# Kernel tuning notes

Measured on AMD Instinct MI355X. Metric: run time of the kernel, lower is better.

## Reference

```python
import jax, jax.numpy as jnp
import numpy as np
import math

H = 768          # bert hidden size
N_HYPO = 384     # number of hyponym instance embeddings
N_HYPER = 384    # number of hypernym instance embeddings
NUM_LABELS = 3


def setup_inputs() -> dict:
    key = jax.random.key(0)
    k1, k2, k3 = jax.random.split(key, 3)
    return {
        "hypo_embeddings": jax.random.normal(k1, (N_HYPO, H), dtype=jnp.float32),
        "hyper_embeddings": jax.random.normal(k2, (N_HYPER, H), dtype=jnp.float32),
        "W_cls": jax.random.normal(k3, (NUM_LABELS, 4 * H), dtype=jnp.float32) * 0.02,
        "b_cls": jnp.zeros((NUM_LABELS,), dtype=jnp.float32),
    }


def reference(hypo_embeddings, hyper_embeddings, W_cls, b_cls):
    h = hypo_embeddings.shape[-1]
    inv_sqrt_h = 1.0 / math.sqrt(h)
    # elementwise outer-product attention score: tanh(x_i * y_j) summed over hidden
    # [n_hypo, n_hyper, h] intermediate -> [n_hypo, n_hyper]
    att = jnp.tanh(hypo_embeddings[:, None, :] * hyper_embeddings[None, :, :]).sum(-1) * inv_sqrt_h

    hypo_side_att = jax.nn.softmax(att, axis=-1)   # rows attend over hypers
    hyper_side_att = jax.nn.softmax(att, axis=0)   # cols attend over hypos

    hyper_typ = hypo_side_att.sum(axis=0)
    hyper_typ = hyper_typ / hyper_typ.sum()
    hypo_typ = hyper_side_att.sum(axis=-1)
    hypo_typ = hypo_typ / hypo_typ.sum()

    # typicalness-weighted prototype pooling
    hyper_prototype = jnp.einsum('nm,md,n->d', hypo_side_att, hyper_embeddings, hypo_typ)
    hypo_prototype = jnp.einsum('nm,nd,m->d', hyper_side_att, hypo_embeddings, hyper_typ)

    feats = jnp.concatenate([
        hyper_prototype,
        hypo_prototype,
        hyper_prototype - hypo_prototype,
        hyper_prototype * hypo_prototype,
    ])  # [4h]
    sub_pred = W_cls @ feats + b_cls  # [num_labels]
    return sub_pred
```

## Files before the change

kernel.cpp:

```cpp
#include <hip/hip_runtime.h>
#include <hip/hip_bf16.h>

#define NN 384
#define HH 768
#define HP 772
#define L2E 1.4426950408889634f
#define TWO_L2E 2.8853900817779268f
#define INV_SQRT_H 0.03608439182435161f

__device__ __forceinline__ float exp2_hw(float x) { return __builtin_amdgcn_exp2f(x); }
__device__ __forceinline__ float rcp_hw(float x) { return __builtin_amdgcn_rcpf(x); }

__global__ __launch_bounds__(256) void k_att(const float* __restrict__ X,
                                             const float* __restrict__ Y,
                                             float* __restrict__ att) {
    __shared__ float xs[8 * HP];
    __shared__ float ys[8 * HP];
    __shared__ float part[4][64];
    const int tid = threadIdx.x;
    const int i0 = blockIdx.y * 8, j0 = blockIdx.x * 8;

    const float4* gx = (const float4*)(X + i0 * HH);
    const float4* gy = (const float4*)(Y + j0 * HH);
#pragma unroll
    for (int p = 0; p < 6; p++) {
        int e = tid + p * 256;
        int r = e / 192, c = e - r * 192;
        float4 vx = gx[e];
        float4 vy = gy[e];
        ((float4*)(xs + r * HP))[c] = vx;
        vy.x *= TWO_L2E; vy.y *= TWO_L2E; vy.z *= TWO_L2E; vy.w *= TWO_L2E;
        ((float4*)(ys + r * HP))[c] = vy;
    }
    __syncthreads();

    const int wv = tid >> 6, ln = tid & 63;
    const int i = ln >> 3, j = ln & 7;
    const float4* xr = (const float4*)(xs + i * HP) + wv * 48;
    const float4* yr = (const float4*)(ys + j * HP) + wv * 48;
    float a0 = 0.f, a1 = 0.f, a2 = 0.f, a3 = 0.f;
#pragma unroll 8
    for (int m = 0; m < 48; m++) {
        float4 a = xr[m];
        float4 b = yr[m];
        a0 += rcp_hw(exp2_hw(a.x * b.x) + 1.f);
        a1 += rcp_hw(exp2_hw(a.y * b.y) + 1.f);
        a2 += rcp_hw(exp2_hw(a.z * b.z) + 1.f);
        a3 += rcp_hw(exp2_hw(a.w * b.w) + 1.f);
    }
    part[wv][ln] = (a0 + a1) + (a2 + a3);
    __syncthreads();
    if (tid < 64) {
        float s = part[0][tid] + part[1][tid] + part[2][tid] + part[3][tid];
        int ii = tid >> 3, jj = tid & 7;
        att[(i0 + ii) * NN + (j0 + jj)] = (768.f - 2.f * s) * INV_SQRT_H;
    }
}

__global__ __launch_bounds__(256) void k_stats(const float* __restrict__ att, float* rowM,
                                               float* rowRS, float* colM, float* colRS) {
    __shared__ float red[4];
    int b = blockIdx.x, t = threadIdx.x;
    bool isRow = b < NN;
    int x = isRow ? b : b - NN;
    float a0 = isRow ? att[x * NN + t] : att[t * NN + x];
    float a1 = (t < 128) ? (isRow ? att[x * NN + t + 256] : att[(t + 256) * NN + x]) : -1e30f;
    float m = fmaxf(a0, a1);
#pragma unroll
    for (int o = 32; o; o >>= 1) m = fmaxf(m, __shfl_xor(m, o, 64));
    if ((t & 63) == 0) red[t >> 6] = m;
    __syncthreads();
    float M = fmaxf(fmaxf(red[0], red[1]), fmaxf(red[2], red[3]));
    __syncthreads();
    float s = exp2_hw((a0 - M) * L2E);
    if (t < 128) s += exp2_hw((a1 - M) * L2E);
#pragma unroll
    for (int o = 32; o; o >>= 1) s += __shfl_xor(s, o, 64);
    if ((t & 63) == 0) red[t >> 6] = s;
    __syncthreads();
    if (t == 0) {
        float S = (red[0] + red[1]) + (red[2] + red[3]);
        if (isRow) { rowM[x] = M; rowRS[x] = 1.f / S; }
        else       { colM[x] = M; colRS[x] = 1.f / S; }
    }
}

__global__ __launch_bounds__(256) void k_typ(const float* __restrict__ att,
                                             const float* __restrict__ rowM,
                                             const float* __restrict__ rowRS,
                                             const float* __restrict__ colM,
                                             const float* __restrict__ colRS,
                                             float* hyper_typ, float* hypo_typ) {
    __shared__ float red[4];
    int b = blockIdx.x, t = threadIdx.x;
    bool isCol = b < NN;
    int x = isCol ? b : b - NN;
    float s = 0.f;
    if (isCol) {
        int j = x;
        for (int i = t; i < NN; i += 256)
            s += exp2_hw((att[i * NN + j] - rowM[i]) * L2E) * rowRS[i];
    } else {
        int i = x;
        for (int j = t; j < NN; j += 256)
            s += exp2_hw((att[i * NN + j] - colM[j]) * L2E) * colRS[j];
    }
#pragma unroll
    for (int o = 32; o; o >>= 1) s += __shfl_xor(s, o, 64);
    if ((t & 63) == 0) red[t >> 6] = s;
    __syncthreads();
    if (t == 0) {
        float S = (red[0] + red[1]) + (red[2] + red[3]);
        if (isCol) hyper_typ[x] = S * (1.f / NN);
        else       hypo_typ[x]  = S * (1.f / NN);
    }
}

__global__ __launch_bounds__(256) void k_w(const float* __restrict__ att,
                                           const float* __restrict__ rowM,
                                           const float* __restrict__ rowRS,
                                           const float* __restrict__ colM,
                                           const float* __restrict__ colRS,
                                           const float* __restrict__ hypo_typ,
                                           const float* __restrict__ hyper_typ,
                                           float* w_hyper, float* w_hypo) {
    __shared__ float red[4];
    int b = blockIdx.x, t = threadIdx.x;
    bool isCol = b < NN;
    int x = isCol ? b : b - NN;
    float s = 0.f;
    if (isCol) {
        int j = x;
        for (int i = t; i < NN; i += 256)
            s += exp2_hw((att[i * NN + j] - rowM[i]) * L2E) * rowRS[i] * hypo_typ[i];
    } else {
        int i = x;
        for (int j = t; j < NN; j += 256)
            s += exp2_hw((att[i * NN + j] - colM[j]) * L2E) * colRS[j] * hyper_typ[j];
    }
#pragma unroll
    for (int o = 32; o; o >>= 1) s += __shfl_xor(s, o, 64);
    if ((t & 63) == 0) red[t >> 6] = s;
    __syncthreads();
    if (t == 0) {
        float S = (red[0] + red[1]) + (red[2] + red[3]);
        if (isCol) w_hyper[x] = S;
        else       w_hypo[x]  = S;
    }
}

__global__ __launch_bounds__(256) void k_proto(const float* __restrict__ X,
                                               const float* __restrict__ Y,
                                               const float* __restrict__ w_hyper,
                                               const float* __restrict__ w_hypo,
                                               float* hp, float* hq) {
    __shared__ float red[4][64];
    int b = blockIdx.x, t = threadIdx.x;
    bool hyper = b < 12;
    int bb = hyper ? b : b - 12;
    int dl = t & 63, w = t >> 6;
    int d = bb * 64 + dl;
    float s = 0.f;
    if (hyper) {
        for (int j = w * 96; j < w * 96 + 96; j++) s += w_hyper[j] * Y[j * HH + d];
    } else {
        for (int i = w * 96; i < w * 96 + 96; i++) s += w_hypo[i] * X[i * HH + d];
    }
    red[w][dl] = s;
    __syncthreads();
    if (t < 64) {
        float S = red[0][t] + red[1][t] + red[2][t] + red[3][t];
        if (hyper) hp[bb * 64 + t] = S;
        else       hq[bb * 64 + t] = S;
    }
}

__global__ __launch_bounds__(256) void k_cls(const float* __restrict__ W,
                                             const float* __restrict__ bias,
                                             const float* __restrict__ hp,
                                             const float* __restrict__ hq,
                                             float* __restrict__ out) {
    __shared__ float red[3][4];
    int t = threadIdx.x;
    float acc0 = 0.f, acc1 = 0.f, acc2 = 0.f;
    for (int d = t; d < 4 * HH; d += 256) {
        int seg = d / HH, r = d - seg * HH;
        float f = (seg == 0) ? hp[r] : (seg == 1) ? hq[r] : (seg == 2) ? (hp[r] - hq[r]) : (hp[r] * hq[r]);
        acc0 += W[d] * f;
        acc1 += W[3072 + d] * f;
        acc2 += W[6144 + d] * f;
    }
#pragma unroll
    for (int o = 32; o; o >>= 1) {
        acc0 += __shfl_xor(acc0, o, 64);
        acc1 += __shfl_xor(acc1, o, 64);
        acc2 += __shfl_xor(acc2, o, 64);
    }
    if ((t & 63) == 0) {
        red[0][t >> 6] = acc0;
        red[1][t >> 6] = acc1;
        red[2][t >> 6] = acc2;
    }
    __syncthreads();
    if (t < 3) {
        float S = red[t][0] + red[t][1] + red[t][2] + red[t][3] + bias[t];
        out[t] = S;
    }
}

extern "C" void kernel_launch(void* const* d_in, const int* in_sizes, int n_in,
                              void* d_out, int out_size, void* d_ws, size_t ws_size,
                              hipStream_t stream) {
    const float* X = (const float*)d_in[0];
    const float* Y = (const float*)d_in[1];
    const float* W = (const float*)d_in[2];
    const float* B = (const float*)d_in[3];
    float* out = (float*)d_out;

    float* ws = (float*)d_ws;
    float* att       = ws;
    float* rowM      = att + NN * NN;
    float* rowRS     = rowM + NN;
    float* colM      = rowRS + NN;
    float* colRS     = colM + NN;
    float* hyper_typ = colRS + NN;
    float* hypo_typ  = hyper_typ + NN;
    float* w_hyper   = hypo_typ + NN;
    float* w_hypo    = w_hyper + NN;
    float* hp        = w_hypo + NN;
    float* hq        = hp + HH;

    k_att<<<dim3(48, 48), 256, 0, stream>>>(X, Y, att);
    k_stats<<<768, 256, 0, stream>>>(att, rowM, rowRS, colM, colRS);
    k_typ<<<768, 256, 0, stream>>>(att, rowM, rowRS, colM, colRS, hyper_typ, hypo_typ);
    k_w<<<768, 256, 0, stream>>>(att, rowM, rowRS, colM, colRS, hypo_typ, hyper_typ, w_hyper, w_hypo);
    k_proto<<<24, 256, 0, stream>>>(X, Y, w_hyper, w_hypo, hp, hq);
    k_cls<<<1, 256, 0, stream>>>(W, B, hp, hq, out);
}
```

Baseline: 103.2 us.

## Fuse post-attention stages into one persistent kernel with grid barriers

Replaces the five kernels after the score computation (stats, typicalness, weights, prototypes, classifier) with a single 384-block kernel that separates phases with atomic-counter grid barriers. The score kernel now also writes a transposed copy of the matrix, so column reductions become contiguous row reads. The aim is to remove four launch gaps and the strided column accesses. In exchange it adds a second full matrix write, relies on all 384 blocks being co-resident for the spin barriers, and resets the barrier counters from one block of the score kernel.

```diff
diff --git a/kernel.cpp b/kernel.cpp
--- a/kernel.cpp
+++ b/kernel.cpp
@@ -13,12 +13,16 @@
 
 __global__ __launch_bounds__(256) void k_att(const float* __restrict__ X,
                                              const float* __restrict__ Y,
-                                             float* __restrict__ att) {
+                                             float* __restrict__ att,
+                                             float* __restrict__ attT,
+                                             unsigned* __restrict__ bar) {
     __shared__ float xs[8 * HP];
     __shared__ float ys[8 * HP];
     __shared__ float part[4][64];
     const int tid = threadIdx.x;
     const int i0 = blockIdx.y * 8, j0 = blockIdx.x * 8;
+
+    if (blockIdx.x == 0 && blockIdx.y == 0) bar[tid] = 0u;
 
     const float4* gx = (const float4*)(X + i0 * HH);
     const float4* gy = (const float4*)(Y + j0 * HH);
@@ -53,158 +57,141 @@
     if (tid < 64) {
         float s = part[0][tid] + part[1][tid] + part[2][tid] + part[3][tid];
         int ii = tid >> 3, jj = tid & 7;
-        att[(i0 + ii) * NN + (j0 + jj)] = (768.f - 2.f * s) * INV_SQRT_H;
-    }
-}
-
-__global__ __launch_bounds__(256) void k_stats(const float* __restrict__ att, float* rowM,
-                                               float* rowRS, float* colM, float* colRS) {
-    __shared__ float red[4];
-    int b = blockIdx.x, t = threadIdx.x;
-    bool isRow = b < NN;
-    int x = isRow ? b : b - NN;
-    float a0 = isRow ? att[x * NN + t] : att[t * NN + x];
-    float a1 = (t < 128) ? (isRow ? att[x * NN + t + 256] : att[(t + 256) * NN + x]) : -1e30f;
-    float m = fmaxf(a0, a1);
+        float v = (768.f - 2.f * s) * INV_SQRT_H;
+        att[(i0 + ii) * NN + (j0 + jj)] = v;
+        attT[(j0 + jj) * NN + (i0 + ii)] = v;
+    }
+}
+
+__device__ __forceinline__ float blk_sum(float v, float* tmp) {
 #pragma unroll
-    for (int o = 32; o; o >>= 1) m = fmaxf(m, __shfl_xor(m, o, 64));
-    if ((t & 63) == 0) red[t >> 6] = m;
-    __syncthreads();
-    float M = fmaxf(fmaxf(red[0], red[1]), fmaxf(red[2], red[3]));
-    __syncthreads();
-    float s = exp2_hw((a0 - M) * L2E);
-    if (t < 128) s += exp2_hw((a1 - M) * L2E);
+    for (int o = 32; o; o >>= 1) v += __shfl_xor(v, o, 64);
+    int t = threadIdx.x;
+    if ((t & 63) == 0) tmp[t >> 6] = v;
+    __syncthreads();
+    float r = (tmp[0] + tmp[1]) + (tmp[2] + tmp[3]);
+    __syncthreads();
+    return r;
+}
+__device__ __forceinline__ float blk_max(float v, float* tmp) {
 #pragma unroll
-    for (int o = 32; o; o >>= 1) s += __shfl_xor(s, o, 64);
-    if ((t & 63) == 0) red[t >> 6] = s;
-    __syncthreads();
-    if (t == 0) {
-        float S = (red[0] + red[1]) + (red[2] + red[3]);
-        if (isRow) { rowM[x] = M; rowRS[x] = 1.f / S; }
-        else       { colM[x] = M; colRS[x] = 1.f / S; }
-    }
-}
-
-__global__ __launch_bounds__(256) void k_typ(const float* __restrict__ att,
-                                             const float* __restrict__ rowM,
-                                             const float* __restrict__ rowRS,
-                                             const float* __restrict__ colM,
-                                             const float* __restrict__ colRS,
-                                             float* hyper_typ, float* hypo_typ) {
-    __shared__ float red[4];
-    int b = blockIdx.x, t = threadIdx.x;
-    bool isCol = b < NN;
-    int x = isCol ? b : b - NN;
-    float s = 0.f;
-    if (isCol) {
-        int j = x;
-        for (int i = t; i < NN; i += 256)
-            s += exp2_hw((att[i * NN + j] - rowM[i]) * L2E) * rowRS[i];
-    } else {
-        int i = x;
-        for (int j = t; j < NN; j += 256)
-            s += exp2_hw((att[i * NN + j] - colM[j]) * L2E) * colRS[j];
-    }
-#pragma unroll
-    for (int o = 32; o; o >>= 1) s += __shfl_xor(s, o, 64);
-    if ((t & 63) == 0) red[t >> 6] = s;
-    __syncthreads();
-    if (t == 0) {
-        float S = (red[0] + red[1]) + (red[2] + red[3]);
-        if (isCol) hyper_typ[x] = S * (1.f / NN);
-        else       hypo_typ[x]  = S * (1.f / NN);
-    }
-}
-
-__global__ __launch_bounds__(256) void k_w(const float* __restrict__ att,
-                                           const float* __restrict__ rowM,
-                                           const float* __restrict__ rowRS,
-                                           const float* __restrict__ colM,
-                                           const float* __restrict__ colRS,
-                                           const float* __restrict__ hypo_typ,
-                                           const float* __restrict__ hyper_typ,
-                                           float* w_hyper, float* w_hypo) {
-    __shared__ float red[4];
-    int b = blockIdx.x, t = threadIdx.x;
-    bool isCol = b < NN;
-    int x = isCol ? b : b - NN;
-    float s = 0.f;
-    if (isCol) {
-        int j = x;
-        for (int i = t; i < NN; i += 256)
-            s += exp2_hw((att[i * NN + j] - rowM[i]) * L2E) * rowRS[i] * hypo_typ[i];
-    } else {
-        int i = x;
-        for (int j = t; j < NN; j += 256)
-            s += exp2_hw((att[i * NN + j] - colM[j]) * L2E) * colRS[j] * hyper_typ[j];
-    }
-#pragma unroll
-    for (int o = 32; o; o >>= 1) s += __shfl_xor(s, o, 64);
-    if ((t & 63) == 0) red[t >> 6] = s;
-    __syncthreads();
-    if (t == 0) {
-        float S = (red[0] + red[1]) + (red[2] + red[3]);
-        if (isCol) w_hyper[x] = S;
-        else       w_hypo[x]  = S;
-    }
-}
-
-__global__ __launch_bounds__(256) void k_proto(const float* __restrict__ X,
-                                               const float* __restrict__ Y,
-                                               const float* __restrict__ w_hyper,
-                                               const float* __restrict__ w_hypo,
-                                               float* hp, float* hq) {
+    for (int o = 32; o; o >>= 1) v = fmaxf(v, __shfl_xor(v, o, 64));
+    int t = threadIdx.x;
+    if ((t & 63) == 0) tmp[t >> 6] = v;
+    __syncthreads();
+    float r = fmaxf(fmaxf(tmp[0], tmp[1]), fmaxf(tmp[2], tmp[3]));
+    __syncthreads();
+    return r;
+}
+
+__device__ __forceinline__ void grid_bar(unsigned* bar, int idx, unsigned nb) {
+    __syncthreads();
+    if (threadIdx.x == 0) {
+        unsigned* cnt = bar + idx * 64;
+        unsigned* flg = cnt + 32;
+        __threadfence();
+        unsigned old = atomicAdd(cnt, 1u);
+        if (old == nb - 1u) {
+            atomicExch(flg, 1u);
+        } else {
+            while (atomicAdd(flg, 0u) == 0u) { __builtin_amdgcn_s_sleep(2); }
+        }
+        __threadfence();
+    }
+    __syncthreads();
+}
+
+__global__ __launch_bounds__(256) void k_tail(const float* __restrict__ att,
+                                              const float* __restrict__ attT,
+                                              const float* __restrict__ X,
+                                              const float* __restrict__ Y,
+                                              const float* __restrict__ W,
+                                              const float* __restrict__ bias,
+                                              float* rowM, float* rowRS, float* colM, float* colRS,
+                                              float* hyper_typ, float* hypo_typ,
+                                              float* w_hyper, float* w_hypo,
+                                              float* hp, float* hq,
+                                              unsigned* bar, float* out) {
+    __shared__ float tmp[4];
     __shared__ float red[4][64];
-    int b = blockIdx.x, t = threadIdx.x;
-    bool hyper = b < 12;
-    int bb = hyper ? b : b - 12;
-    int dl = t & 63, w = t >> 6;
-    int d = bb * 64 + dl;
-    float s = 0.f;
-    if (hyper) {
-        for (int j = w * 96; j < w * 96 + 96; j++) s += w_hyper[j] * Y[j * HH + d];
-    } else {
-        for (int i = w * 96; i < w * 96 + 96; i++) s += w_hypo[i] * X[i * HH + d];
-    }
-    red[w][dl] = s;
-    __syncthreads();
-    if (t < 64) {
-        float S = red[0][t] + red[1][t] + red[2][t] + red[3][t];
-        if (hyper) hp[bb * 64 + t] = S;
-        else       hq[bb * 64 + t] = S;
-    }
-}
-
-__global__ __launch_bounds__(256) void k_cls(const float* __restrict__ W,
-                                             const float* __restrict__ bias,
-                                             const float* __restrict__ hp,
-                                             const float* __restrict__ hq,
-                                             float* __restrict__ out) {
-    __shared__ float red[3][4];
-    int t = threadIdx.x;
-    float acc0 = 0.f, acc1 = 0.f, acc2 = 0.f;
-    for (int d = t; d < 4 * HH; d += 256) {
-        int seg = d / HH, r = d - seg * HH;
-        float f = (seg == 0) ? hp[r] : (seg == 1) ? hq[r] : (seg == 2) ? (hp[r] - hq[r]) : (hp[r] * hq[r]);
-        acc0 += W[d] * f;
-        acc1 += W[3072 + d] * f;
-        acc2 += W[6144 + d] * f;
-    }
-#pragma unroll
-    for (int o = 32; o; o >>= 1) {
-        acc0 += __shfl_xor(acc0, o, 64);
-        acc1 += __shfl_xor(acc1, o, 64);
-        acc2 += __shfl_xor(acc2, o, 64);
-    }
-    if ((t & 63) == 0) {
-        red[0][t >> 6] = acc0;
-        red[1][t >> 6] = acc1;
-        red[2][t >> 6] = acc2;
-    }
-    __syncthreads();
-    if (t < 3) {
-        float S = red[t][0] + red[t][1] + red[t][2] + red[t][3] + bias[t];
-        out[t] = S;
+    const int b = blockIdx.x, t = threadIdx.x;
+    const unsigned nb = gridDim.x;
+
+    {
+        float a0 = att[b * NN + t];
+        float a1 = (t < 128) ? att[b * NN + 256 + t] : -1e30f;
+        float M = blk_max(fmaxf(a0, a1), tmp);
+        float s = exp2_hw((a0 - M) * L2E) + ((t < 128) ? exp2_hw((a1 - M) * L2E) : 0.f);
+        float S = blk_sum(s, tmp);
+        if (t == 0) { rowM[b] = M; rowRS[b] = 1.f / S; }
+
+        float c0 = attT[b * NN + t];
+        float c1 = (t < 128) ? attT[b * NN + 256 + t] : -1e30f;
+        float Mc = blk_max(fmaxf(c0, c1), tmp);
+        float sc = exp2_hw((c0 - Mc) * L2E) + ((t < 128) ? exp2_hw((c1 - Mc) * L2E) : 0.f);
+        float Sc = blk_sum(sc, tmp);
+        if (t == 0) { colM[b] = Mc; colRS[b] = 1.f / Sc; }
+    }
+    grid_bar(bar, 0, nb);
+
+    {
+        float s1 = 0.f, s2 = 0.f;
+        for (int i = t; i < NN; i += 256) s1 += exp2_hw((attT[b * NN + i] - rowM[i]) * L2E) * rowRS[i];
+        for (int j = t; j < NN; j += 256) s2 += exp2_hw((att[b * NN + j] - colM[j]) * L2E) * colRS[j];
+        float S1 = blk_sum(s1, tmp);
+        float S2 = blk_sum(s2, tmp);
+        if (t == 0) { hyper_typ[b] = S1 * (1.f / NN); hypo_typ[b] = S2 * (1.f / NN); }
+    }
+    grid_bar(bar, 1, nb);
+
+    {
+        float u1 = 0.f, u2 = 0.f;
+        for (int i = t; i < NN; i += 256) u1 += exp2_hw((attT[b * NN + i] - rowM[i]) * L2E) * rowRS[i] * hypo_typ[i];
+        for (int j = t; j < NN; j += 256) u2 += exp2_hw((att[b * NN + j] - colM[j]) * L2E) * colRS[j] * hyper_typ[j];
+        float U1 = blk_sum(u1, tmp);
+        float U2 = blk_sum(u2, tmp);
+        if (t == 0) { w_hyper[b] = U1; w_hypo[b] = U2; }
+    }
+    grid_bar(bar, 2, nb);
+
+    if (b < 24) {
+        bool hyper = b < 12;
+        int bb = hyper ? b : b - 12;
+        int dl = t & 63, w = t >> 6;
+        int d = bb * 64 + dl;
+        float s = 0.f;
+        if (hyper) {
+            for (int j = w * 96; j < w * 96 + 96; j++) s += w_hyper[j] * Y[j * HH + d];
+        } else {
+            for (int i = w * 96; i < w * 96 + 96; i++) s += w_hypo[i] * X[i * HH + d];
+        }
+        red[w][dl] = s;
+        __syncthreads();
+        if (t < 64) {
+            float S = red[0][t] + red[1][t] + red[2][t] + red[3][t];
+            if (hyper) hp[bb * 64 + t] = S;
+            else       hq[bb * 64 + t] = S;
+        }
+    }
+    grid_bar(bar, 3, nb);
+
+    if (b == 0) {
+        float acc0 = 0.f, acc1 = 0.f, acc2 = 0.f;
+        for (int d = t; d < 4 * HH; d += 256) {
+            int seg = d / HH, r = d - seg * HH;
+            float f = (seg == 0) ? hp[r] : (seg == 1) ? hq[r] : (seg == 2) ? (hp[r] - hq[r]) : (hp[r] * hq[r]);
+            acc0 += W[d] * f;
+            acc1 += W[3072 + d] * f;
+            acc2 += W[6144 + d] * f;
+        }
+        float A0 = blk_sum(acc0, tmp);
+        float A1 = blk_sum(acc1, tmp);
+        float A2 = blk_sum(acc2, tmp);
+        if (t == 0) {
+            out[0] = A0 + bias[0];
+            out[1] = A1 + bias[1];
+            out[2] = A2 + bias[2];
+        }
     }
 }
 
@@ -219,7 +206,8 @@
 
     float* ws = (float*)d_ws;
     float* att       = ws;
-    float* rowM      = att + NN * NN;
+    float* attT      = att + NN * NN;
+    float* rowM      = attT + NN * NN;
     float* rowRS     = rowM + NN;
     float* colM      = rowRS + NN;
     float* colRS     = colM + NN;
@@ -229,11 +217,11 @@
     float* w_hypo    = w_hyper + NN;
     float* hp        = w_hypo + NN;
     float* hq        = hp + HH;
-
-    k_att<<<dim3(48, 48), 256, 0, stream>>>(X, Y, att);
-    k_stats<<<768, 256, 0, stream>>>(att, rowM, rowRS, colM, colRS);
-    k_typ<<<768, 256, 0, stream>>>(att, rowM, rowRS, colM, colRS, hyper_typ, hypo_typ);
-    k_w<<<768, 256, 0, stream>>>(att, rowM, rowRS, colM, colRS, hypo_typ, hyper_typ, w_hyper, w_hypo);
-    k_proto<<<24, 256, 0, stream>>>(X, Y, w_hyper, w_hypo, hp, hq);
-    k_cls<<<1, 256, 0, stream>>>(W, B, hp, hq, out);
-}
+    unsigned* bar    = (unsigned*)(hq + HH);
+
+    k_att<<<dim3(48, 48), 256, 0, stream>>>(X, Y, att, attT, bar);
+    k_tail<<<384, 256, 0, stream>>>(att, attT, X, Y, W, B,
+                                    rowM, rowRS, colM, colRS,
+                                    hyper_typ, hypo_typ, w_hyper, w_hypo,
+                                    hp, hq, bar, out);
+}
```

Result: slower. 149.7 us (+45.0%).
